# Kernel tuning notes

Hardware: AMD Instinct MI355X
Metric: run time of the kernel (lower is better)

## Reference

```python
import jax, jax.numpy as jnp
import numpy as np

N, D = 8192, 1024
TEMPERATURE = 0.1
EPS = 1e-8

def setup_inputs() -> dict:
    key = jax.random.key(0)
    k1, k2 = jax.random.split(key)
    emb = jax.random.normal(k1, (N, D), dtype=jnp.float32)
    # docstring: embeddings are normalized
    emb = emb / jnp.linalg.norm(emb, axis=1, keepdims=True)
    labels = jax.random.randint(k2, (N,), 0, 2, dtype=jnp.int32)
    return {"embeddings": emb, "labels": labels}

def reference(embeddings, labels):
    lab = labels.astype(embeddings.dtype)            # (N,)
    sim = jnp.matmul(embeddings, embeddings.T) / TEMPERATURE  # (N, N)
    exp_sim = jnp.exp(sim)                           # original uses raw exp (no max-subtract)
    diag = jnp.diagonal(exp_sim)                     # self-similarity exp(1/T)
    # all_sim excludes self; pos_sim = other reference rows (labels==1, j != i)
    all_sum = exp_sim.sum(axis=1) - diag             # (N,)
    pos_sum = exp_sim @ lab - diag * lab             # subtract self only when i is ref
    loss_per_row = -jnp.log(pos_sum / (all_sum + EPS))
    n_ref = lab.sum()
    loss = jnp.sum(jnp.where(lab > 0, loss_per_row, 0.0)) / jnp.maximum(n_ref, 1.0)
    # original returns 0.0 when fewer than 2 reference rows
    return jnp.where(n_ref < 2, jnp.array(0.0, embeddings.dtype), loss)
```

## Files before the change

### kernel.cpp

```cpp
#include <hip/hip_runtime.h>
#include <hip/hip_bf16.h>
#include <cstdint>
#include <cstddef>

#define NROWS 8192
#define DIM   1024
#define BMR 128
#define BNC 128
#define BK  64
#define NBLK 2080
#define EPS 1e-8f
#define PRESCALE 3.798288f

typedef short  bf16x8  __attribute__((ext_vector_type(8)));
typedef float  floatx4 __attribute__((ext_vector_type(4)));

typedef __attribute__((address_space(1))) const void CGV;
typedef __attribute__((address_space(3))) void LV;

__device__ __forceinline__ void async_load16(const void* g, void* l) {
    __builtin_amdgcn_global_load_lds((CGV*)g, (LV*)l, 16, 0, 0);
}

__device__ __forceinline__ unsigned short f2bf_rne(float f) {
    union { float f; unsigned u; } c; c.f = f;
    unsigned u = c.u;
    unsigned r = (u + 0x7fffu + ((u >> 16) & 1u)) >> 16;
    return (unsigned short)r;
}

__global__ __launch_bounds__(256) void convert_kernel(
    const float* __restrict__ in, unsigned short* __restrict__ out,
    float* __restrict__ accum )
{
    int i = (blockIdx.x * 256 + threadIdx.x) * 4;
    float4 v = *(const float4*)(in + i);
    ushort4 o;
    o.x = f2bf_rne(v.x * PRESCALE);
    o.y = f2bf_rne(v.y * PRESCALE);
    o.z = f2bf_rne(v.z * PRESCALE);
    o.w = f2bf_rne(v.w * PRESCALE);
    *(ushort4*)(out + i) = o;
    if (blockIdx.x < (2 * NROWS) / 256)
        accum[blockIdx.x * 256 + threadIdx.x] = 0.0f;
}

__global__ __launch_bounds__(128, 2) void gemm_fused_kernel(
    const unsigned short* __restrict__ E,
    const int*            __restrict__ labels,
    float*                __restrict__ all_sum,
    float*                __restrict__ pos_sum)
{
    __shared__ __align__(16) unsigned short sA[BMR * BK];
    __shared__ __align__(16) unsigned short sB[BNC * BK];

    const int tid  = threadIdx.x;
    const int lane = tid & 63;
    const int w    = tid >> 6;
    const int colw = lane & 15;
    const int quad = lane >> 4;

    const int b = blockIdx.x;
    const int t = (b & 7) * 260 + (b >> 3);
    int bi = (int)((sqrtf(8.0f * (float)t + 1.0f) - 1.0f) * 0.5f);
    while ((bi + 1) * (bi + 2) / 2 <= t) ++bi;
    while (bi * (bi + 1) / 2 > t) --bi;
    const int bj = t - bi * (bi + 1) / 2;

    const int rBase = bi * BMR;
    const int cBase = bj * BNC;

    const int srow = tid >> 3;
    const int scol = (((tid & 7) ^ (srow & 7)) << 3);
    const int e0   = tid * 8;

    floatx4 acc[4][8];
    #pragma unroll
    for (int i = 0; i < 4; ++i)
        #pragma unroll
        for (int j = 0; j < 8; ++j)
            acc[i][j] = (floatx4)0.0f;

    const int swz   = colw & 7;
    const int aRow0 = (w * 64 + colw) * BK;
    const int bRow0 = colw * BK;

    const size_t gA0 = (size_t)(rBase + srow) * DIM + scol;
    const size_t gB0 = (size_t)(cBase + srow) * DIM + scol;
    const size_t rstep = (size_t)16 * DIM;

    for (int k0 = 0; k0 < DIM; k0 += BK) {
        __syncthreads();
        #pragma unroll
        for (int j = 0; j < 8; ++j)
            async_load16(E + gA0 + j * rstep + k0, &sA[e0 + j * 1024]);
        #pragma unroll
        for (int j = 0; j < 8; ++j)
            async_load16(E + gB0 + j * rstep + k0, &sB[e0 + j * 1024]);
        __syncthreads();

        #pragma unroll
        for (int h = 0; h < 2; ++h) {
            const int cOff = (((h << 2) | quad) ^ swz) << 3;
            bf16x8 aF[4], bF[8];
            #pragma unroll
            for (int mt = 0; mt < 4; ++mt)
                aF[mt] = *(const bf16x8*)&sA[aRow0 + mt * 16 * BK + cOff];
            #pragma unroll
            for (int nt = 0; nt < 8; ++nt)
                bF[nt] = *(const bf16x8*)&sB[bRow0 + nt * 16 * BK + cOff];

            #pragma unroll
            for (int mt = 0; mt < 4; ++mt)
                #pragma unroll
                for (int nt = 0; nt < 8; ++nt)
                    acc[mt][nt] = __builtin_amdgcn_mfma_f32_16x16x32_bf16(
                        aF[mt], bF[nt], acc[mt][nt], 0, 0, 0);
        }
    }

    float labc[8];
    int   gcol[8];
    #pragma unroll
    for (int nt = 0; nt < 8; ++nt) {
        gcol[nt] = cBase + nt * 16 + colw;
        labc[nt] = (float)labels[gcol[nt]];
    }

    float colAll[8] = {0.f, 0.f, 0.f, 0.f, 0.f, 0.f, 0.f, 0.f};
    float colPos[8] = {0.f, 0.f, 0.f, 0.f, 0.f, 0.f, 0.f, 0.f};

    #pragma unroll
    for (int mt = 0; mt < 4; ++mt) {
        const int growBase = rBase + w * 64 + mt * 16 + quad * 4;
        #pragma unroll
        for (int r = 0; r < 4; ++r) {
            const int grow = growBase + r;
            const float labr = (float)labels[grow];
            float sAll = 0.f, sPos = 0.f;
            #pragma unroll
            for (int nt = 0; nt < 8; ++nt) {
                float ev = exp2f(acc[mt][nt][r]);
                ev = (grow > gcol[nt]) ? ev : 0.0f;
                sAll += ev;
                sPos += ev * labc[nt];
                colAll[nt] += ev;
                colPos[nt] += ev * labr;
            }
            #pragma unroll
            for (int off = 1; off < 16; off <<= 1) {
                sAll += __shfl_xor(sAll, off);
                sPos += __shfl_xor(sPos, off);
            }
            if (colw == 0 && sAll != 0.f) {
                atomicAdd(&all_sum[grow], sAll);
                atomicAdd(&pos_sum[grow], sPos);
            }
        }
    }

    #pragma unroll
    for (int nt = 0; nt < 8; ++nt) {
        float a = colAll[nt], p = colPos[nt];
        a += __shfl_xor(a, 16);  p += __shfl_xor(p, 16);
        a += __shfl_xor(a, 32);  p += __shfl_xor(p, 32);
        if (quad == 0 && a != 0.f) {
            atomicAdd(&all_sum[gcol[nt]], a);
            atomicAdd(&pos_sum[gcol[nt]], p);
        }
    }
}

__global__ __launch_bounds__(1024) void finalize_kernel(
    const float* __restrict__ all_sum,
    const float* __restrict__ pos_sum,
    const int*   __restrict__ labels,
    float*       __restrict__ out)
{
    __shared__ float sSum[1024];
    __shared__ float sCnt[1024];
    const int tid = threadIdx.x;
    float lsum = 0.f, lcnt = 0.f;
    for (int i = tid; i < NROWS; i += 1024) {
        if (labels[i] > 0) {
            float p = pos_sum[i];
            float a = all_sum[i] + EPS;
            lsum += -logf(p / a);
            lcnt += 1.0f;
        }
    }
    sSum[tid] = lsum;
    sCnt[tid] = lcnt;
    __syncthreads();
    for (int s = 512; s > 0; s >>= 1) {
        if (tid < s) { sSum[tid] += sSum[tid + s]; sCnt[tid] += sCnt[tid + s]; }
        __syncthreads();
    }
    if (tid == 0) {
        float n = sCnt[0];
        out[0] = (n < 2.0f) ? 0.0f : sSum[0] / fmaxf(n, 1.0f);
    }
}

extern "C" void kernel_launch(void* const* d_in, const int* in_sizes, int n_in,
                              void* d_out, int out_size, void* d_ws, size_t ws_size,
                              hipStream_t stream) {
    const float* emb    = (const float*)d_in[0];
    const int*   labels = (const int*)d_in[1];
    float*       out    = (float*)d_out;

    unsigned short* Ebf = (unsigned short*)d_ws;
    const size_t embBytes = (size_t)NROWS * DIM * sizeof(unsigned short);
    float* all_sum = (float*)((char*)d_ws + embBytes);
    float* pos_sum = all_sum + NROWS;

    convert_kernel<<<(NROWS * DIM) / (4 * 256), 256, 0, stream>>>(emb, Ebf, all_sum);

    gemm_fused_kernel<<<NBLK, 128, 0, stream>>>(Ebf, labels, all_sum, pos_sum);

    finalize_kernel<<<1, 1024, 0, stream>>>(all_sum, pos_sum, labels, out);
}
```

Measured before the change: 183.6 us.

## Use 256x128 tiles with 8 waves and triple-buffered async LDS pipeline

Restructures the fused GEMM to 256x128 block tiles over a rectangular lower-triangle schedule, with 512 threads (8 waves in a 4x2 layout), BK=32 and a three-stage LDS ring buffer. Global-to-LDS async loads are issued two stages ahead, and explicit waitcnt and barriers replace the per-iteration double syncthreads, so memory latency overlaps MFMA work. Block count drops and tiles become taller, which adds more redundant above-diagonal compute per tile. It also relies on correct manual vmcnt accounting.

```diff
diff --git a/kernel.cpp b/kernel.cpp
--- a/kernel.cpp
+++ b/kernel.cpp
@@ -5,12 +5,16 @@
 
 #define NROWS 8192
 #define DIM   1024
-#define BMR 128
+#define BMR 256
 #define BNC 128
-#define BK  64
-#define NBLK 2080
+#define BK  32
+#define NKS (DIM / BK)
+#define NBLK 1056
 #define EPS 1e-8f
 #define PRESCALE 3.798288f
+
+#define ABUF 8192
+#define BUFE 12288
 
 typedef short  bf16x8  __attribute__((ext_vector_type(8)));
 typedef float  floatx4 __attribute__((ext_vector_type(4)));
@@ -45,103 +49,119 @@
         accum[blockIdx.x * 256 + threadIdx.x] = 0.0f;
 }
 
-__global__ __launch_bounds__(128, 2) void gemm_fused_kernel(
+__global__ __launch_bounds__(512, 4) void gemm_fused_kernel(
     const unsigned short* __restrict__ E,
     const int*            __restrict__ labels,
     float*                __restrict__ all_sum,
     float*                __restrict__ pos_sum)
 {
-    __shared__ __align__(16) unsigned short sA[BMR * BK];
-    __shared__ __align__(16) unsigned short sB[BNC * BK];
+    __shared__ __align__(16) unsigned short S[3 * BUFE];
 
     const int tid  = threadIdx.x;
     const int lane = tid & 63;
     const int w    = tid >> 6;
+    const int wm   = w >> 1;
+    const int wn   = w & 1;
     const int colw = lane & 15;
     const int quad = lane >> 4;
 
     const int b = blockIdx.x;
-    const int t = (b & 7) * 260 + (b >> 3);
-    int bi = (int)((sqrtf(8.0f * (float)t + 1.0f) - 1.0f) * 0.5f);
-    while ((bi + 1) * (bi + 2) / 2 <= t) ++bi;
-    while (bi * (bi + 1) / 2 > t) --bi;
-    const int bj = t - bi * (bi + 1) / 2;
-
-    const int rBase = bi * BMR;
-    const int cBase = bj * BNC;
-
-    const int srow = tid >> 3;
-    const int scol = (((tid & 7) ^ (srow & 7)) << 3);
-    const int e0   = tid * 8;
-
-    floatx4 acc[4][8];
+    const int t = (b & 7) * 132 + (b >> 3);
+    int a = (int)((sqrtf(4.0f * (float)t + 1.0f) - 1.0f) * 0.5f);
+    while ((a + 1) * (a + 2) <= t) ++a;
+    while (a * (a + 1) > t) --a;
+    const int c = t - a * (a + 1);
+
+    const int rBase = a * BMR;
+    const int cBase = c * BNC;
+
+    const int l4  = lane >> 2;
+    const int gch = (lane & 3) ^ (l4 & 3);
+    const unsigned short* gA0 = E + (size_t)(rBase + w * 32 + l4) * DIM + gch * 8;
+    const unsigned short* gA1 = gA0 + (size_t)16 * DIM;
+    const unsigned short* gB  = E + (size_t)(cBase + w * 16 + l4) * DIM + gch * 8;
+    const int aL0 = (w * 128 + lane) * 8;
+    const int bL  = (w * 64 + lane) * 8;
+
+    const int fs    = (quad ^ (colw & 3)) * 8;
+    const int aBase = (wm * 64 + colw) * BK + fs;
+    const int bBase = (wn * 64 + colw) * BK + fs;
+
+    floatx4 acc[4][4];
     #pragma unroll
     for (int i = 0; i < 4; ++i)
         #pragma unroll
-        for (int j = 0; j < 8; ++j)
+        for (int j = 0; j < 4; ++j)
             acc[i][j] = (floatx4)0.0f;
 
-    const int swz   = colw & 7;
-    const int aRow0 = (w * 64 + colw) * BK;
-    const int bRow0 = colw * BK;
-
-    const size_t gA0 = (size_t)(rBase + srow) * DIM + scol;
-    const size_t gB0 = (size_t)(cBase + srow) * DIM + scol;
-    const size_t rstep = (size_t)16 * DIM;
-
-    for (int k0 = 0; k0 < DIM; k0 += BK) {
-        __syncthreads();
-        #pragma unroll
-        for (int j = 0; j < 8; ++j)
-            async_load16(E + gA0 + j * rstep + k0, &sA[e0 + j * 1024]);
-        #pragma unroll
-        for (int j = 0; j < 8; ++j)
-            async_load16(E + gB0 + j * rstep + k0, &sB[e0 + j * 1024]);
-        __syncthreads();
-
-        #pragma unroll
-        for (int h = 0; h < 2; ++h) {
-            const int cOff = (((h << 2) | quad) ^ swz) << 3;
-            bf16x8 aF[4], bF[8];
+#define STAGE(T, SB) do { \
+        async_load16(gA0 + (T) * BK, &S[(SB) * BUFE + aL0]);        \
+        async_load16(gA1 + (T) * BK, &S[(SB) * BUFE + aL0 + 512]);  \
+        async_load16(gB  + (T) * BK, &S[(SB) * BUFE + ABUF + bL]);  \
+    } while (0)
+
+    STAGE(0, 0);
+    STAGE(1, 1);
+    asm volatile("s_waitcnt vmcnt(3)" ::: "memory");
+    __builtin_amdgcn_s_barrier();
+    __builtin_amdgcn_sched_barrier(0);
+
+    #pragma unroll
+    for (int kt = 0; kt < NKS; ++kt) {
+        const int rb = kt % 3;
+        const int sb = (kt + 2) % 3;
+
+        bf16x8 bF[4];
+        #pragma unroll
+        for (int nt = 0; nt < 4; ++nt)
+            bF[nt] = *(const bf16x8*)&S[rb * BUFE + ABUF + bBase + nt * 16 * BK];
+
+        if (kt < NKS - 2) STAGE(kt + 2, sb);
+
+        __builtin_amdgcn_s_setprio(1);
+        #pragma unroll
+        for (int mt = 0; mt < 4; ++mt) {
+            bf16x8 aF = *(const bf16x8*)&S[rb * BUFE + aBase + mt * 16 * BK];
             #pragma unroll
-            for (int mt = 0; mt < 4; ++mt)
-                aF[mt] = *(const bf16x8*)&sA[aRow0 + mt * 16 * BK + cOff];
-            #pragma unroll
-            for (int nt = 0; nt < 8; ++nt)
-                bF[nt] = *(const bf16x8*)&sB[bRow0 + nt * 16 * BK + cOff];
-
-            #pragma unroll
-            for (int mt = 0; mt < 4; ++mt)
-                #pragma unroll
-                for (int nt = 0; nt < 8; ++nt)
-                    acc[mt][nt] = __builtin_amdgcn_mfma_f32_16x16x32_bf16(
-                        aF[mt], bF[nt], acc[mt][nt], 0, 0, 0);
-        }
-    }
-
-    float labc[8];
-    int   gcol[8];
-    #pragma unroll
-    for (int nt = 0; nt < 8; ++nt) {
-        gcol[nt] = cBase + nt * 16 + colw;
-        labc[nt] = (float)labels[gcol[nt]];
-    }
-
-    float colAll[8] = {0.f, 0.f, 0.f, 0.f, 0.f, 0.f, 0.f, 0.f};
-    float colPos[8] = {0.f, 0.f, 0.f, 0.f, 0.f, 0.f, 0.f, 0.f};
+            for (int nt = 0; nt < 4; ++nt)
+                acc[mt][nt] = __builtin_amdgcn_mfma_f32_16x16x32_bf16(
+                    aF, bF[nt], acc[mt][nt], 0, 0, 0);
+        }
+        __builtin_amdgcn_s_setprio(0);
+
+        __builtin_amdgcn_sched_barrier(0);
+        if (kt < NKS - 2)
+            asm volatile("s_waitcnt vmcnt(3) lgkmcnt(0)" ::: "memory");
+        else
+            asm volatile("s_waitcnt vmcnt(0) lgkmcnt(0)" ::: "memory");
+        __builtin_amdgcn_s_barrier();
+        __builtin_amdgcn_sched_barrier(0);
+    }
+#undef STAGE
+
+    float labc[4];
+    int   gcolv[4];
+    #pragma unroll
+    for (int nt = 0; nt < 4; ++nt) {
+        gcolv[nt] = cBase + wn * 64 + nt * 16 + colw;
+        labc[nt]  = (float)labels[gcolv[nt]];
+    }
+
+    float colAll[4] = {0.f, 0.f, 0.f, 0.f};
+    float colPos[4] = {0.f, 0.f, 0.f, 0.f};
 
     #pragma unroll
     for (int mt = 0; mt < 4; ++mt) {
-        const int growBase = rBase + w * 64 + mt * 16 + quad * 4;
+        const int growBase = rBase + wm * 64 + mt * 16 + quad * 4;
         #pragma unroll
         for (int r = 0; r < 4; ++r) {
             const int grow = growBase + r;
             const float labr = (float)labels[grow];
             float sAll = 0.f, sPos = 0.f;
             #pragma unroll
-            for (int nt = 0; nt < 8; ++nt) {
+            for (int nt = 0; nt < 4; ++nt) {
                 float ev = exp2f(acc[mt][nt][r]);
-                ev = (grow > gcol[nt]) ? ev : 0.0f;
+                ev = (grow > gcolv[nt]) ? ev : 0.0f;
                 sAll += ev;
                 sPos += ev * labc[nt];
                 colAll[nt] += ev;
@@ -160,13 +180,13 @@
     }
 
     #pragma unroll
-    for (int nt = 0; nt < 8; ++nt) {
-        float a = colAll[nt], p = colPos[nt];
-        a += __shfl_xor(a, 16);  p += __shfl_xor(p, 16);
-        a += __shfl_xor(a, 32);  p += __shfl_xor(p, 32);
-        if (quad == 0 && a != 0.f) {
-            atomicAdd(&all_sum[gcol[nt]], a);
-            atomicAdd(&pos_sum[gcol[nt]], p);
+    for (int nt = 0; nt < 4; ++nt) {
+        float aa = colAll[nt], p = colPos[nt];
+        aa += __shfl_xor(aa, 16);  p += __shfl_xor(p, 16);
+        aa += __shfl_xor(aa, 32);  p += __shfl_xor(p, 32);
+        if (quad == 0 && aa != 0.f) {
+            atomicAdd(&all_sum[gcolv[nt]], aa);
+            atomicAdd(&pos_sum[gcolv[nt]], p);
         }
     }
 }
@@ -216,7 +236,7 @@
 
     convert_kernel<<<(NROWS * DIM) / (4 * 256), 256, 0, stream>>>(emb, Ebf, all_sum);
 
-    gemm_fused_kernel<<<NBLK, 128, 0, stream>>>(Ebf, labels, all_sum, pos_sum);
+    gemm_fused_kernel<<<NBLK, 512, 0, stream>>>(Ebf, labels, all_sum, pos_sum);
 
     finalize_kernel<<<1, 1024, 0, stream>>>(all_sum, pos_sum, labels, out);
 }
```

After: 190.4 us. 1.04x slower.

## Use single-wave 128x128 tiles with double-buffered async LDS prefetch

Applied to the files above, without the earlier changes.

The GEMM block shrinks from two waves to one wave of 64 threads. That single wave computes the full 128x128 tile with an 8x8 MFMA accumulator grid, which doubles the fragment reuse per wave. LDS is now double-buffered: the next K-tile is issued via global_load_lds before the current one is computed, and vmcnt waits replace the __syncthreads barriers. This aims to hide global load latency and remove block-level syncs. The costs are a large accumulator register footprint (256 VGPRs of acc), 64KB of LDS per block, and much lower wave occupancy per CU.

```diff
diff --git a/kernel.cpp b/kernel.cpp
--- a/kernel.cpp
+++ b/kernel.cpp
@@ -5,12 +5,15 @@
 
 #define NROWS 8192
 #define DIM   1024
-#define BMR 128
-#define BNC 128
-#define BK  64
-#define NBLK 2080
+#define BT    128
+#define BK    64
+#define NKT   (DIM / BK)
+#define NBLK  2080
 #define EPS 1e-8f
 #define PRESCALE 3.798288f
+
+#define ABUF_E 8192
+#define BUF_E  16384
 
 typedef short  bf16x8  __attribute__((ext_vector_type(8)));
 typedef float  floatx4 __attribute__((ext_vector_type(4)));
@@ -45,20 +48,18 @@
         accum[blockIdx.x * 256 + threadIdx.x] = 0.0f;
 }
 
-__global__ __launch_bounds__(128, 2) void gemm_fused_kernel(
+__global__ __launch_bounds__(64, 1) void gemm_fused_kernel(
     const unsigned short* __restrict__ E,
     const int*            __restrict__ labels,
     float*                __restrict__ all_sum,
     float*                __restrict__ pos_sum)
 {
-    __shared__ __align__(16) unsigned short sA[BMR * BK];
-    __shared__ __align__(16) unsigned short sB[BNC * BK];
-
-    const int tid  = threadIdx.x;
-    const int lane = tid & 63;
-    const int w    = tid >> 6;
+    __shared__ __align__(16) unsigned short S[2 * BUF_E];
+
+    const int lane = threadIdx.x;
     const int colw = lane & 15;
     const int quad = lane >> 4;
+    const int swz  = colw & 7;
 
     const int b = blockIdx.x;
     const int t = (b & 7) * 260 + (b >> 3);
@@ -67,57 +68,68 @@
     while (bi * (bi + 1) / 2 > t) --bi;
     const int bj = t - bi * (bi + 1) / 2;
 
-    const int rBase = bi * BMR;
-    const int cBase = bj * BNC;
-
-    const int srow = tid >> 3;
-    const int scol = (((tid & 7) ^ (srow & 7)) << 3);
-    const int e0   = tid * 8;
-
-    floatx4 acc[4][8];
-    #pragma unroll
-    for (int i = 0; i < 4; ++i)
+    const int rBase = bi * BT;
+    const int cBase = bj * BT;
+
+    const int l8  = lane >> 3;
+    const int gch = (lane & 7) ^ l8;
+    const unsigned short* gA = E + (size_t)(rBase + l8) * DIM + gch * 8;
+    const unsigned short* gB = E + (size_t)(cBase + l8) * DIM + gch * 8;
+    const int ldsT = lane * 8;
+
+#define STAGE(T, SB) do {                                                     \
+        const size_t _gk = (size_t)(T) * BK;                                  \
+        _Pragma("unroll")                                                     \
+        for (int j = 0; j < 16; ++j) {                                        \
+            async_load16(gA + (size_t)j * (8 * DIM) + _gk,                    \
+                         &S[(SB) * BUF_E + j * 512 + ldsT]);                  \
+            async_load16(gB + (size_t)j * (8 * DIM) + _gk,                    \
+                         &S[(SB) * BUF_E + ABUF_E + j * 512 + ldsT]);         \
+        }                                                                     \
+    } while (0)
+
+    floatx4 acc[8][8];
+    #pragma unroll
+    for (int i = 0; i < 8; ++i)
         #pragma unroll
         for (int j = 0; j < 8; ++j)
             acc[i][j] = (floatx4)0.0f;
 
-    const int swz   = colw & 7;
-    const int aRow0 = (w * 64 + colw) * BK;
-    const int bRow0 = colw * BK;
-
-    const size_t gA0 = (size_t)(rBase + srow) * DIM + scol;
-    const size_t gB0 = (size_t)(cBase + srow) * DIM + scol;
-    const size_t rstep = (size_t)16 * DIM;
-
-    for (int k0 = 0; k0 < DIM; k0 += BK) {
-        __syncthreads();
+    STAGE(0, 0);
+
+    for (int kt = 0; kt < NKT; ++kt) {
+        if (kt < NKT - 1) {
+            STAGE(kt + 1, (kt + 1) & 1);
+            asm volatile("s_waitcnt vmcnt(32)" ::: "memory");
+        } else {
+            asm volatile("s_waitcnt vmcnt(0)" ::: "memory");
+        }
+        __builtin_amdgcn_sched_barrier(0);
+
+        const int bb = (kt & 1) * BUF_E;
         #pragma unroll
-        for (int j = 0; j < 8; ++j)
-            async_load16(E + gA0 + j * rstep + k0, &sA[e0 + j * 1024]);
-        #pragma unroll
-        for (int j = 0; j < 8; ++j)
-            async_load16(E + gB0 + j * rstep + k0, &sB[e0 + j * 1024]);
-        __syncthreads();
-
-        #pragma unroll
-        for (int h = 0; h < 2; ++h) {
-            const int cOff = (((h << 2) | quad) ^ swz) << 3;
-            bf16x8 aF[4], bF[8];
-            #pragma unroll
-            for (int mt = 0; mt < 4; ++mt)
-                aF[mt] = *(const bf16x8*)&sA[aRow0 + mt * 16 * BK + cOff];
+        for (int ksub = 0; ksub < 2; ++ksub) {
+            const int cs = (((ksub << 2) | quad) ^ swz) << 3;
+            bf16x8 aF[8], bF[8];
             #pragma unroll
             for (int nt = 0; nt < 8; ++nt)
-                bF[nt] = *(const bf16x8*)&sB[bRow0 + nt * 16 * BK + cOff];
-
-            #pragma unroll
-            for (int mt = 0; mt < 4; ++mt)
+                bF[nt] = *(const bf16x8*)&S[bb + ABUF_E +
+                              (nt * 16 + colw) * BK + cs];
+            #pragma unroll
+            for (int mt = 0; mt < 8; ++mt)
+                aF[mt] = *(const bf16x8*)&S[bb + (mt * 16 + colw) * BK + cs];
+            #pragma unroll
+            for (int mt = 0; mt < 8; ++mt)
                 #pragma unroll
                 for (int nt = 0; nt < 8; ++nt)
                     acc[mt][nt] = __builtin_amdgcn_mfma_f32_16x16x32_bf16(
                         aF[mt], bF[nt], acc[mt][nt], 0, 0, 0);
         }
-    }
+
+        asm volatile("s_waitcnt lgkmcnt(0)" ::: "memory");
+        __builtin_amdgcn_sched_barrier(0);
+    }
+#undef STAGE
 
     float labc[8];
     int   gcol[8];
@@ -131,8 +143,8 @@
     float colPos[8] = {0.f, 0.f, 0.f, 0.f, 0.f, 0.f, 0.f, 0.f};
 
     #pragma unroll
-    for (int mt = 0; mt < 4; ++mt) {
-        const int growBase = rBase + w * 64 + mt * 16 + quad * 4;
+    for (int mt = 0; mt < 8; ++mt) {
+        const int growBase = rBase + mt * 16 + quad * 4;
         #pragma unroll
         for (int r = 0; r < 4; ++r) {
             const int grow = growBase + r;
@@ -216,7 +228,7 @@
 
     convert_kernel<<<(NROWS * DIM) / (4 * 256), 256, 0, stream>>>(emb, Ebf, all_sum);
 
-    gemm_fused_kernel<<<NBLK, 128, 0, stream>>>(Ebf, labels, all_sum, pos_sum);
+    gemm_fused_kernel<<<NBLK, 64, 0, stream>>>(Ebf, labels, all_sum, pos_sum);
 
     finalize_kernel<<<1, 1024, 0, stream>>>(all_sum, pos_sum, labels, out);
 }
```

Result: slower. 337.8 us (+84.0%).
